# Optimization experiments

Hardware: AMD Instinct MI355X
Metric: run time of the kernel (lower is better)

Reference implementation:

```python
import jax, jax.numpy as jnp
import numpy as np
from jax import lax

N_CLASS, EMB, HID = 32000, 512, 1024
BATCH, SEQ = 64, 256


def _run_lstm(xs, h0, c0, Wg, Wgh, bg, Wi, Wih, bi, Wf, Wfh, bf, Wo, Woh, bo):
    # xs: [T, B, D_in]; weights stored [D_in, H] so step is x @ W (== Linear)
    def step(carry, x):
        h, c = carry
        g = jnp.tanh(x @ Wg + h @ Wgh + bg)
        i = jax.nn.sigmoid(x @ Wi + h @ Wih + bi)
        f = jax.nn.sigmoid(x @ Wf + h @ Wfh + bf)
        o = jax.nn.sigmoid(x @ Wo + h @ Woh + bo)
        c = c * f + g * i
        h = jnp.tanh(c) * o
        return (h, c), h
    (hT, cT), hs = lax.scan(step, (h0, c0), xs)
    return hs, hT


def setup_inputs() -> dict:
    key = jax.random.key(0)
    ks = jax.random.split(key, 32)
    s_e, s_h = 1.0 / np.sqrt(EMB), 1.0 / np.sqrt(HID)
    d = {}
    d["X"] = jax.random.randint(ks[0], (BATCH, SEQ), 0, N_CLASS)
    d["C"] = jax.random.normal(ks[1], (N_CLASS, EMB), jnp.float32)
    # layer 1 (input dim EMB)
    names1 = ["W1", "W_xi", "W_xf", "W_xo"]
    names1h = ["W2", "W_hi", "W_hf", "W_ho"]
    for j, n in enumerate(names1):
        d[n] = jax.random.normal(ks[2 + j], (EMB, HID), jnp.float32) * s_e
    for j, n in enumerate(names1h):
        d[n] = jax.random.normal(ks[6 + j], (HID, HID), jnp.float32) * s_h
    for n in ["b1", "b_i", "b_f", "b_o"]:
        d[n] = jnp.ones((HID,), jnp.float32)
    # layer 2 (input dim HID)
    names2 = ["W1_y", "W_xi_y", "W_xf_y", "W_xo_y", "W2_y", "W_hi_y", "W_hf_y", "W_ho_y"]
    for j, n in enumerate(names2):
        d[n] = jax.random.normal(ks[10 + j], (HID, HID), jnp.float32) * s_h
    for n in ["b1_y", "b_i_y", "b_f_y", "b_o_y"]:
        d[n] = jnp.ones((HID,), jnp.float32)
    d["W3"] = jax.random.normal(ks[20], (HID, N_CLASS), jnp.float32) * s_h
    d["b2"] = jnp.ones((N_CLASS,), jnp.float32)
    # torch code uses torch.randn initial states each call; materialize them
    d["h0"] = jax.random.normal(ks[21], (BATCH, HID), jnp.float32)
    d["c0"] = jax.random.normal(ks[22], (BATCH, HID), jnp.float32)
    d["h0_y"] = jax.random.normal(ks[23], (BATCH, HID), jnp.float32)
    d["c0_y"] = jax.random.normal(ks[24], (BATCH, HID), jnp.float32)
    return d


def reference(X, C, W1, W_xi, W_xf, W_xo, W2, W_hi, W_hf, W_ho,
              b1, b_i, b_f, b_o,
              W1_y, W_xi_y, W_xf_y, W_xo_y, W2_y, W_hi_y, W_hf_y, W_ho_y,
              b1_y, b_i_y, b_f_y, b_o_y, W3, b2, h0, c0, h0_y, c0_y):
    xs = jnp.transpose(C[X], (1, 0, 2))  # [T, B, EMB]
    hs, _ = _run_lstm(xs, h0, c0, W1, W2, b1, W_xi, W_hi, b_i,
                      W_xf, W_hf, b_f, W_xo, W_ho, b_o)
    _, hT_y = _run_lstm(hs, h0_y, c0_y, W1_y, W2_y, b1_y, W_xi_y, W_hi_y, b_i_y,
                        W_xf_y, W_hf_y, b_f_y, W_xo_y, W_ho_y, b_o_y)
    return hT_y @ W3 + b2  # [B, N_CLASS]
```

## Files before the change

kernel.cpp:

```cpp
#include <hip/hip_runtime.h>
#include <hip/hip_bf16.h>


typedef __attribute__((ext_vector_type(8))) short s16x8;
typedef __attribute__((ext_vector_type(4))) float f32x4;
typedef unsigned long long u64;

#define N_CLASS 32000
#define EMB 512
#define HID 1024
#define BATCH 64
#define SEQ 256
#define NG4 4096

#define PIN(v) asm volatile("" : "+v"(v))

static __device__ __forceinline__ short f2bf(float x) {
  __hip_bfloat16 h = __float2bfloat16(x);
  return *reinterpret_cast<short*>(&h);
}
static __device__ __forceinline__ float bf2f(short x) {
  __hip_bfloat16 h = *reinterpret_cast<__hip_bfloat16*>(&x);
  return __bfloat162float(h);
}
static __device__ __forceinline__ float fsigm(float x) {
  return __builtin_amdgcn_rcpf(1.f + __expf(-x));
}
static __device__ __forceinline__ float ftanh(float x) {
  return 2.f * __builtin_amdgcn_rcpf(1.f + __expf(-2.f * x)) - 1.f;
}

__global__ void k_conv_w4(const float* __restrict__ Wg, const float* __restrict__ Wi,
                          const float* __restrict__ Wf, const float* __restrict__ Wo,
                          short* __restrict__ sw, int K) {
  int i = blockIdx.x * 256 + threadIdx.x;
  int k8 = i >> 10, j = i & 1023;
  if (k8 >= (K >> 3)) return;
  const float* W = blockIdx.z == 0 ? Wg : blockIdx.z == 1 ? Wi : blockIdx.z == 2 ? Wf : Wo;
  s16x8 v;
#pragma unroll
  for (int e = 0; e < 8; ++e) v[e] = f2bf(W[(size_t)(k8 * 8 + e) * 1024 + j]);
  *(s16x8*)(sw + ((size_t)k8 * NG4 + blockIdx.z * 1024 + j) * 8) = v;
}

__global__ void k_bcat(const float* __restrict__ b0, const float* __restrict__ b1,
                       const float* __restrict__ b2, const float* __restrict__ b3,
                       float* __restrict__ dst) {
  int i = blockIdx.x * 256 + threadIdx.x;
  const float* s = (i >> 10) == 0 ? b0 : (i >> 10) == 1 ? b1 : (i >> 10) == 2 ? b2 : b3;
  dst[i] = s[i & 1023];
}

__global__ void k_f2bf(const float* __restrict__ src, short* __restrict__ dst, int n) {
  int i = blockIdx.x * 256 + threadIdx.x;
  if (i < n) dst[i] = f2bf(src[i]);
}

__global__ void k_embed(const int* __restrict__ X, const float* __restrict__ C,
                        short* __restrict__ xs) {
  int r = blockIdx.x;
  int t = r >> 6, b = r & 63;
  int idx = X[b * SEQ + t];
  const float* src = C + (size_t)idx * EMB;
  float2 v = *(const float2*)(src + threadIdx.x * 2);
  short* dst = xs + (size_t)r * EMB + threadIdx.x * 2;
  dst[0] = f2bf(v.x);
  dst[1] = f2bf(v.y);
}

__global__ __launch_bounds__(256) void k_gemx(const short* __restrict__ A,
                                              const short* __restrict__ Bsw,
                                              const float* __restrict__ bias,
                                              u64* __restrict__ Gsw) {
  __shared__ short lds[4096 * 8];
  int tid = threadIdx.x;
  int n0 = blockIdx.x * 64;
  for (int cid = tid; cid < 4096; cid += 256) {
    int k8 = cid >> 6, nl = cid & 63;
    *(s16x8*)(lds + (size_t)cid * 8) = *(const s16x8*)(Bsw + ((size_t)k8 * NG4 + n0 + nl) * 8);
  }
  __syncthreads();
  int lane = tid & 63, wid = tid >> 6;
  int l15 = lane & 15, l4 = lane >> 4;
  int ms = wid >> 1, ns = wid & 1;
  for (int m0 = blockIdx.y * 64; m0 < SEQ * BATCH; m0 += gridDim.y * 64) {
    f32x4 acc[2][2];
#pragma unroll
    for (int i = 0; i < 2; ++i)
#pragma unroll
      for (int j = 0; j < 2; ++j) acc[i][j] = (f32x4){0.f, 0.f, 0.f, 0.f};
    const short* a0p = A + (size_t)(m0 + ms * 32 + l15) * EMB + l4 * 8;
    const short* a1p = a0p + (size_t)16 * EMB;
#pragma unroll 4
    for (int kc = 0; kc < 16; ++kc) {
      s16x8 av0 = *(const s16x8*)(a0p + kc * 32);
      s16x8 av1 = *(const s16x8*)(a1p + kc * 32);
#pragma unroll
      for (int j = 0; j < 2; ++j) {
        s16x8 bv = *(const s16x8*)(lds + (size_t)((kc * 4 + l4) * 64 + ns * 32 + j * 16 + l15) * 8);
        acc[0][j] = __builtin_amdgcn_mfma_f32_16x16x32_bf16(av0, bv, acc[0][j], 0, 0, 0);
        acc[1][j] = __builtin_amdgcn_mfma_f32_16x16x32_bf16(av1, bv, acc[1][j], 0, 0, 0);
      }
    }
    int t = m0 >> 6;
#pragma unroll
    for (int i = 0; i < 2; ++i)
#pragma unroll
      for (int j = 0; j < 2; ++j) {
        int grp = ms * 2 + i;
        int colg = n0 + ns * 32 + j * 16 + l15;
        float bv = bias[colg];
        int q = colg >> 10, nslc = (colg >> 4) & 63;
        u64 pk = 0;
#pragma unroll
        for (int e = 0; e < 4; ++e)
          pk |= (u64)(unsigned short)f2bf(acc[i][j][e] + bv) << (16 * e);
        size_t slot = ((((size_t)t * 4 + grp) * 64 + nslc) * 4 + q) * 64 + l4 * 16 + l15;
        Gsw[slot] = pk;
      }
  }
}

__global__ __launch_bounds__(512) __attribute__((amdgpu_waves_per_eu(2, 2))) void k_mega(
    const u64* __restrict__ G64, const short* __restrict__ Wh1sw,
    const short* __restrict__ Wx2sw, const short* __restrict__ Wh2sw,
    const float* __restrict__ bc2, u64* __restrict__ h1ex, u64* __restrict__ h2ex,
    const float* __restrict__ c0, const float* __restrict__ c0y,
    u64* __restrict__ hTy, unsigned* __restrict__ flags) {
  __shared__ short a_lds[2 * 16 * 1024];
  __shared__ f32x4 xch[8][64];
  const int tid = threadIdx.x;
  const int lane = tid & 63, W = tid >> 6;
  const int wv = W & 3, khalf = W >> 2;
  const int l15 = lane & 15, l4 = lane >> 4;
  const int xcd = (int)blockIdx.x & 7;
  const int group = xcd >> 1;
  const int nsl = ((((int)blockIdx.x >> 3) << 1) | (xcd & 1));
  const int col = (l15 >> 2) * 1024 + nsl * 16 + wv * 4 + (l15 & 3);

  s16x8 b1r[16], bxr[16], b2r[16];
#pragma unroll
  for (int j = 0; j < 16; ++j) {
    size_t o = ((size_t)((khalf * 16 + j) * 4 + l4) * NG4 + col) * 8;
    b1r[j] = *(const s16x8*)(Wh1sw + o);
    PIN(b1r[j]);
  }
#pragma unroll
  for (int j = 0; j < 16; ++j) {
    size_t o = ((size_t)((khalf * 16 + j) * 4 + l4) * NG4 + col) * 8;
    bxr[j] = *(const s16x8*)(Wx2sw + o);
    PIN(bxr[j]);
  }
#pragma unroll
  for (int j = 0; j < 16; ++j) {
    size_t o = ((size_t)((khalf * 16 + j) * 4 + l4) * NG4 + col) * 8;
    b2r[j] = *(const s16x8*)(Wh2sw + o);
    PIN(b2r[j]);
  }
  const float bias2 = bc2[col];
  float cv[4];
#pragma unroll
  for (int e = 0; e < 4; ++e) {
    int gi = (group * 16 + l4 * 4 + e) * HID + nsl * 16 + wv * 4 + (l15 & 3);
    cv[e] = (W < 4 ? c0 : c0y)[gi];
  }
  unsigned* arr = flags;
  const int srow = tid >> 5, sc5 = tid & 31;
  const int exrow = (group * 16 + srow) * 256;
  const size_t gbase =
      (((size_t)group * 64 + nsl) * 4 + (l15 >> 2)) * 64 + l4 * 16 + wv * 4 + (l15 & 3);
  u64 gcur = (W < 4) ? G64[gbase] : 0;
  u64 gnext = 0;
  const int gsrc = l4 * 16 + (l15 & 3);
  const int psrc = ((l15 >> 2) << 4) + ((l15 & 3) << 2);
  const int swzm = (l15 & 7) << 4;
  const int abase = l15 * 2048 + khalf * 1024 + l4 * 16;

  for (int r = 0; r <= 256; ++r) {
    if (W < 4 && r + 1 < 256) gnext = G64[gbase + (size_t)(r + 1) * 65536];
    if (r > 0) {
      if (tid < 64) {
        unsigned* p = arr + ((group << 6) + tid) * 32;
        while (__hip_atomic_load(p, __ATOMIC_RELAXED, __HIP_MEMORY_SCOPE_AGENT) <
               (unsigned)r) {
        }
      }
      __syncthreads();
      asm volatile("" ::: "memory");
    }
    {
      const int slot = (r + 1) & 1;
      const u64* s1 = h1ex + slot * 16384 + exrow;
      const u64* s2 = h2ex + slot * 16384 + exrow;
#pragma unroll
      for (int i = 0; i < 8; ++i) {
        int chunk = sc5 + (i << 5);
        u64 v1 = __hip_atomic_load(s1 + chunk, __ATOMIC_RELAXED, __HIP_MEMORY_SCOPE_AGENT);
        u64 v2 = __hip_atomic_load(s2 + chunk, __ATOMIC_RELAXED, __HIP_MEMORY_SCOPE_AGENT);
        int bo = (srow * 2048 + chunk * 8) ^ ((srow & 7) << 4);
        *(u64*)((char*)a_lds + bo) = v1;
        *(u64*)((char*)a_lds + 32768 + bo) = v2;
      }
    }
    __syncthreads();

    f32x4 p1, p2a, p2b;
    if (W < 4) {
#pragma unroll
      for (int e = 0; e < 4; ++e)
        p1[e] = __uint_as_float((unsigned)((gcur >> (16 * e)) & 0xffffu) << 16);
      p2a = (f32x4){0.f, 0.f, 0.f, 0.f};
    } else {
      p1 = (f32x4){0.f, 0.f, 0.f, 0.f};
      p2a = (f32x4){bias2, bias2, bias2, bias2};
    }
    p2b = (f32x4){0.f, 0.f, 0.f, 0.f};
#pragma unroll
    for (int j = 0; j < 16; ++j) {
      int o = (abase + j * 64) ^ swzm;
      s16x8 a1 = *(const s16x8*)((const char*)a_lds + o);
      s16x8 a2 = *(const s16x8*)((const char*)a_lds + 32768 + o);
      p1 = __builtin_amdgcn_mfma_f32_16x16x32_bf16(a1, b1r[j], p1, 0, 0, 0);
      p2a = __builtin_amdgcn_mfma_f32_16x16x32_bf16(a1, bxr[j], p2a, 0, 0, 0);
      p2b = __builtin_amdgcn_mfma_f32_16x16x32_bf16(a2, b2r[j], p2b, 0, 0, 0);
    }
    f32x4 p2 = p2a + p2b;
    if (W < 4) {
      if (r >= 1) xch[W][lane] = p2;
    } else {
      if (r < 256) xch[W][lane] = p1;
    }
    __syncthreads();

    if (W < 4) {
      if (r < 256) {
        f32x4 po = xch[W + 4][lane];
        f32x4 acc = p1 + po;
        float hh0, hh1, hh2, hh3;
#pragma unroll
        for (int e = 0; e < 4; ++e) {
          float xg = __shfl(acc[e], gsrc + 0);
          float xi = __shfl(acc[e], gsrc + 4);
          float xf = __shfl(acc[e], gsrc + 8);
          float xo = __shfl(acc[e], gsrc + 12);
          float cn = cv[e] * fsigm(xf) + ftanh(xg) * fsigm(xi);
          cv[e] = cn;
          float hv = ftanh(cn) * fsigm(xo);
          if (e == 0) hh0 = hv;
          else if (e == 1) hh1 = hv;
          else if (e == 2) hh2 = hv;
          else hh3 = hv;
        }
        int rr = l15 >> 2;
        float hexp = rr == 0 ? hh0 : rr == 1 ? hh1 : rr == 2 ? hh2 : hh3;
        float p0 = __shfl(hexp, psrc + 0);
        float p1s = __shfl(hexp, psrc + 1);
        float p2s = __shfl(hexp, psrc + 2);
        float p3s = __shfl(hexp, psrc + 3);
        if (lane < 16) {
          u64 pk = (u64)(unsigned short)f2bf(p0) | ((u64)(unsigned short)f2bf(p1s) << 16) |
                   ((u64)(unsigned short)f2bf(p2s) << 32) |
                   ((u64)(unsigned short)f2bf(p3s) << 48);
          __hip_atomic_store(
              h1ex + (r & 1) * 16384 + (group * 16 + lane) * 256 + nsl * 4 + wv, pk,
              __ATOMIC_RELAXED, __HIP_MEMORY_SCOPE_AGENT);
        }
      }
    } else {
      if (r >= 1) {
        f32x4 po = xch[W - 4][lane];
        f32x4 acc = p2 + po;
        float hh0, hh1, hh2, hh3;
#pragma unroll
        for (int e = 0; e < 4; ++e) {
          float xg = __shfl(acc[e], gsrc + 0);
          float xi = __shfl(acc[e], gsrc + 4);
          float xf = __shfl(acc[e], gsrc + 8);
          float xo = __shfl(acc[e], gsrc + 12);
          float cn = cv[e] * fsigm(xf) + ftanh(xg) * fsigm(xi);
          cv[e] = cn;
          float hv = ftanh(cn) * fsigm(xo);
          if (e == 0) hh0 = hv;
          else if (e == 1) hh1 = hv;
          else if (e == 2) hh2 = hv;
          else hh3 = hv;
        }
        int rr = l15 >> 2;
        float hexp = rr == 0 ? hh0 : rr == 1 ? hh1 : rr == 2 ? hh2 : hh3;
        float p0 = __shfl(hexp, psrc + 0);
        float p1s = __shfl(hexp, psrc + 1);
        float p2s = __shfl(hexp, psrc + 2);
        float p3s = __shfl(hexp, psrc + 3);
        if (lane < 16) {
          u64 pk = (u64)(unsigned short)f2bf(p0) | ((u64)(unsigned short)f2bf(p1s) << 16) |
                   ((u64)(unsigned short)f2bf(p2s) << 32) |
                   ((u64)(unsigned short)f2bf(p3s) << 48);
          int idx = (group * 16 + lane) * 256 + nsl * 4 + wv;
          if (r < 256)
            __hip_atomic_store(h2ex + (r & 1) * 16384 + idx, pk, __ATOMIC_RELAXED,
                               __HIP_MEMORY_SCOPE_AGENT);
          else
            hTy[idx] = pk;
        }
      }
    }

    if (r < 256) {
      asm volatile("s_waitcnt vmcnt(0)" ::: "memory");
      __syncthreads();
      if (tid == 0)
        __hip_atomic_store(arr + ((group << 6) + nsl) * 32, (unsigned)(r + 1),
                           __ATOMIC_RELAXED, __HIP_MEMORY_SCOPE_AGENT);
    }
    gcur = gnext;
  }
}

__global__ __launch_bounds__(256) void k_final(const short* __restrict__ hT,
                                               const float* __restrict__ W3,
                                               float* __restrict__ partial) {
  __shared__ float hst[64][64];
  int tid = threadIdx.x;
  int n = blockIdx.x * 256 + tid;
  int kbase = blockIdx.y * 512;
  float acc[64];
#pragma unroll
  for (int i = 0; i < 64; ++i) acc[i] = 0.f;
  int bb = tid >> 2, part = tid & 3;
  for (int kc = 0; kc < 512; kc += 64) {
    __syncthreads();
    s16x8 v0 = *(const s16x8*)(hT + bb * HID + kbase + kc + part * 16);
    s16x8 v1 = *(const s16x8*)(hT + bb * HID + kbase + kc + part * 16 + 8);
#pragma unroll
    for (int e = 0; e < 8; ++e) {
      hst[part * 16 + e][bb] = bf2f(v0[e]);
      hst[part * 16 + 8 + e][bb] = bf2f(v1[e]);
    }
    __syncthreads();
    for (int k = 0; k < 64; ++k) {
      float wv = W3[(size_t)(kbase + kc + k) * N_CLASS + n];
      const float4* hp = (const float4*)&hst[k][0];
#pragma unroll
      for (int b4 = 0; b4 < 16; ++b4) {
        float4 h4 = hp[b4];
        acc[b4 * 4 + 0] += h4.x * wv;
        acc[b4 * 4 + 1] += h4.y * wv;
        acc[b4 * 4 + 2] += h4.z * wv;
        acc[b4 * 4 + 3] += h4.w * wv;
      }
    }
  }
#pragma unroll
  for (int b = 0; b < 64; ++b)
    partial[((size_t)blockIdx.y * 64 + b) * N_CLASS + n] = acc[b];
}

__global__ void k_fincomb(const float* __restrict__ partial, const float* __restrict__ b2,
                          float* __restrict__ out) {
  int n = blockIdx.x * 256 + threadIdx.x;
  int b = blockIdx.y;
  out[(size_t)b * N_CLASS + n] =
      partial[(size_t)b * N_CLASS + n] + partial[((size_t)64 + b) * N_CLASS + n] + b2[n];
}

extern "C" void kernel_launch(void* const* d_in, const int* in_sizes, int n_in, void* d_out,
                              int out_size, void* d_ws, size_t ws_size, hipStream_t stream) {
  (void)in_sizes; (void)n_in; (void)out_size; (void)ws_size;
  const int* X = (const int*)d_in[0];
  const float* C = (const float*)d_in[1];
  const float* W1 = (const float*)d_in[2];
  const float* W_xi = (const float*)d_in[3];
  const float* W_xf = (const float*)d_in[4];
  const float* W_xo = (const float*)d_in[5];
  const float* W2 = (const float*)d_in[6];
  const float* W_hi = (const float*)d_in[7];
  const float* W_hf = (const float*)d_in[8];
  const float* W_ho = (const float*)d_in[9];
  const float* b1 = (const float*)d_in[10];
  const float* b_i = (const float*)d_in[11];
  const float* b_f = (const float*)d_in[12];
  const float* b_o = (const float*)d_in[13];
  const float* W1_y = (const float*)d_in[14];
  const float* W_xi_y = (const float*)d_in[15];
  const float* W_xf_y = (const float*)d_in[16];
  const float* W_xo_y = (const float*)d_in[17];
  const float* W2_y = (const float*)d_in[18];
  const float* W_hi_y = (const float*)d_in[19];
  const float* W_hf_y = (const float*)d_in[20];
  const float* W_ho_y = (const float*)d_in[21];
  const float* b1_y = (const float*)d_in[22];
  const float* b_i_y = (const float*)d_in[23];
  const float* b_f_y = (const float*)d_in[24];
  const float* b_o_y = (const float*)d_in[25];
  const float* W3 = (const float*)d_in[26];
  const float* b2 = (const float*)d_in[27];
  const float* h0 = (const float*)d_in[28];
  const float* c0 = (const float*)d_in[29];
  const float* h0_y = (const float*)d_in[30];
  const float* c0_y = (const float*)d_in[31];

  char* w = (char*)d_ws;
  size_t off = 0;
  auto take = [&](size_t bytes) {
    char* p = w + off;
    off += (bytes + 255) & ~(size_t)255;
    return p;
  };
  short* wx1 = (short*)take(64UL * NG4 * 8 * 2);
  short* wh1 = (short*)take(128UL * NG4 * 8 * 2);
  short* wx2 = (short*)take(128UL * NG4 * 8 * 2);
  short* wh2 = (short*)take(128UL * NG4 * 8 * 2);
  short* xs = (short*)take((size_t)SEQ * BATCH * EMB * 2);
  u64* G1sw = (u64*)take((size_t)SEQ * 65536 * 8);
  float* bc1 = (float*)take(NG4 * 4);
  float* bc2 = (float*)take(NG4 * 4);
  u64* h1ex = (u64*)take(2UL * 16384 * 8);
  u64* h2ex = (u64*)take(2UL * 16384 * 8);
  u64* hTy = (u64*)take(16384UL * 8);
  unsigned* flags = (unsigned*)take(65536);

  hipMemsetAsync(flags, 0, 65536, stream);
  k_bcat<<<16, 256, 0, stream>>>(b1, b_i, b_f, b_o, bc1);
  k_bcat<<<16, 256, 0, stream>>>(b1_y, b_i_y, b_f_y, b_o_y, bc2);
  k_f2bf<<<256, 256, 0, stream>>>(h0, (short*)h1ex + 65536, BATCH * HID);
  k_f2bf<<<256, 256, 0, stream>>>(h0_y, (short*)h2ex, BATCH * HID);
  k_conv_w4<<<dim3(256, 1, 4), 256, 0, stream>>>(W1, W_xi, W_xf, W_xo, wx1, 512);
  k_conv_w4<<<dim3(512, 1, 4), 256, 0, stream>>>(W2, W_hi, W_hf, W_ho, wh1, 1024);
  k_conv_w4<<<dim3(512, 1, 4), 256, 0, stream>>>(W1_y, W_xi_y, W_xf_y, W_xo_y, wx2, 1024);
  k_conv_w4<<<dim3(512, 1, 4), 256, 0, stream>>>(W2_y, W_hi_y, W_hf_y, W_ho_y, wh2, 1024);
  k_embed<<<SEQ * BATCH, 256, 0, stream>>>(X, C, xs);
  k_gemx<<<dim3(64, 16), 256, 0, stream>>>(xs, wx1, bc1, G1sw);
  k_mega<<<256, 512, 0, stream>>>(G1sw, wh1, wx2, wh2, bc2, h1ex, h2ex, c0, c0_y, hTy,
                                  flags);
  float* partial = (float*)G1sw;
  k_final<<<dim3(125, 2), 256, 0, stream>>>((const short*)hTy, W3, partial);
  k_fincomb<<<dim3(125, 64), 256, 0, stream>>>(partial, b2, (float*)d_out);
}
```

Measured before the change: 2.443 ms.

## Split LSTM layers into decoupled wave groups with separate flag pipelines

Restructures the persistent recurrent kernel so layer 1 and layer 2 run on separate wave groups (4 waves for layer 1, 8 for layer 2) with their own global step flags. They synchronise through LDS atomic counters instead of block-wide barriers, so layer 2 can lag layer 1 and the two recurrences pipeline. Each wave now holds the full K=1024 weight slice for one gate in registers and gate math is done per element with LDS exchange. This adds spin-wait complexity, higher register pressure at 768 threads, and a risk of ordering bugs between the LDS counters and global flags.

```diff
diff --git a/kernel.cpp b/kernel.cpp
--- a/kernel.cpp
+++ b/kernel.cpp
@@ -28,6 +28,17 @@
 }
 static __device__ __forceinline__ float ftanh(float x) {
   return 2.f * __builtin_amdgcn_rcpf(1.f + __expf(-2.f * x)) - 1.f;
+}
+static __device__ __forceinline__ u64 pack4(float a, float b, float c, float d) {
+  return (u64)(unsigned short)f2bf(a) | ((u64)(unsigned short)f2bf(b) << 16) |
+         ((u64)(unsigned short)f2bf(c) << 32) | ((u64)(unsigned short)f2bf(d) << 48);
+}
+static __device__ __forceinline__ void wgadd(unsigned* c) {
+  __hip_atomic_fetch_add(c, 1u, __ATOMIC_RELEASE, __HIP_MEMORY_SCOPE_WORKGROUP);
+}
+static __device__ __forceinline__ void wgwait(unsigned* c, unsigned tgt) {
+  while (__hip_atomic_load(c, __ATOMIC_ACQUIRE, __HIP_MEMORY_SCOPE_WORKGROUP) < tgt) {
+  }
 }
 
 __global__ void k_conv_w4(const float* __restrict__ Wg, const float* __restrict__ Wi,
@@ -121,198 +132,206 @@
   }
 }
 
-__global__ __launch_bounds__(512) __attribute__((amdgpu_waves_per_eu(2, 2))) void k_mega(
+__global__ __launch_bounds__(768) __attribute__((amdgpu_waves_per_eu(3))) void k_mega(
     const u64* __restrict__ G64, const short* __restrict__ Wh1sw,
     const short* __restrict__ Wx2sw, const short* __restrict__ Wh2sw,
     const float* __restrict__ bc2, u64* __restrict__ h1ex, u64* __restrict__ h2ex,
     const float* __restrict__ c0, const float* __restrict__ c0y,
     u64* __restrict__ hTy, unsigned* __restrict__ flags) {
-  __shared__ short a_lds[2 * 16 * 1024];
-  __shared__ f32x4 xch[8][64];
+  __shared__ short A1[16 * 1024];
+  __shared__ float gx1[4][16][16];
+  __shared__ short B1[16 * 1024];
+  __shared__ short B2[16 * 1024];
+  __shared__ float xch2[2][4][16][16];
+  __shared__ unsigned cnt[16];
+
   const int tid = threadIdx.x;
   const int lane = tid & 63, W = tid >> 6;
-  const int wv = W & 3, khalf = W >> 2;
-  const int l15 = lane & 15, l4 = lane >> 4;
   const int xcd = (int)blockIdx.x & 7;
   const int group = xcd >> 1;
   const int nsl = ((((int)blockIdx.x >> 3) << 1) | (xcd & 1));
-  const int col = (l15 >> 2) * 1024 + nsl * 16 + wv * 4 + (l15 & 3);
-
-  s16x8 b1r[16], bxr[16], b2r[16];
-#pragma unroll
-  for (int j = 0; j < 16; ++j) {
-    size_t o = ((size_t)((khalf * 16 + j) * 4 + l4) * NG4 + col) * 8;
-    b1r[j] = *(const s16x8*)(Wh1sw + o);
-    PIN(b1r[j]);
-  }
-#pragma unroll
-  for (int j = 0; j < 16; ++j) {
-    size_t o = ((size_t)((khalf * 16 + j) * 4 + l4) * NG4 + col) * 8;
-    bxr[j] = *(const s16x8*)(Wx2sw + o);
-    PIN(bxr[j]);
-  }
-#pragma unroll
-  for (int j = 0; j < 16; ++j) {
-    size_t o = ((size_t)((khalf * 16 + j) * 4 + l4) * NG4 + col) * 8;
-    b2r[j] = *(const s16x8*)(Wh2sw + o);
-    PIN(b2r[j]);
-  }
-  const float bias2 = bc2[col];
-  float cv[4];
-#pragma unroll
-  for (int e = 0; e < 4; ++e) {
-    int gi = (group * 16 + l4 * 4 + e) * HID + nsl * 16 + wv * 4 + (l15 & 3);
-    cv[e] = (W < 4 ? c0 : c0y)[gi];
-  }
-  unsigned* arr = flags;
-  const int srow = tid >> 5, sc5 = tid & 31;
-  const int exrow = (group * 16 + srow) * 256;
-  const size_t gbase =
-      (((size_t)group * 64 + nsl) * 4 + (l15 >> 2)) * 64 + l4 * 16 + wv * 4 + (l15 & 3);
-  u64 gcur = (W < 4) ? G64[gbase] : 0;
-  u64 gnext = 0;
-  const int gsrc = l4 * 16 + (l15 & 3);
-  const int psrc = ((l15 >> 2) << 4) + ((l15 & 3) << 2);
+  if (tid < 16) cnt[tid] = 0u;
+  __syncthreads();
+
+  unsigned* flags1 = flags;
+  unsigned* flags2 = flags + 8192;
+  const int l15 = lane & 15, l4 = lane >> 4;
+  const int abase = l15 * 2048 + l4 * 16;
   const int swzm = (l15 & 7) << 4;
-  const int abase = l15 * 2048 + khalf * 1024 + l4 * 16;
-
-  for (int r = 0; r <= 256; ++r) {
-    if (W < 4 && r + 1 < 256) gnext = G64[gbase + (size_t)(r + 1) * 65536];
-    if (r > 0) {
-      if (tid < 64) {
-        unsigned* p = arr + ((group << 6) + tid) * 32;
-        while (__hip_atomic_load(p, __ATOMIC_RELAXED, __HIP_MEMORY_SCOPE_AGENT) <
-               (unsigned)r) {
+
+  if (W < 4) {
+    const int q = W;
+    s16x8 b1r[32];
+#pragma unroll
+    for (int j = 0; j < 32; ++j) {
+      b1r[j] = *(const s16x8*)(Wh1sw + ((size_t)(j * 4 + l4) * NG4 + q * 1024 + nsl * 16 + l15) * 8);
+      PIN(b1r[j]);
+    }
+    const int b_ = tid >> 4, d_ = tid & 15;
+    float c1 = c0[(group * 16 + b_) * HID + nsl * 16 + d_];
+    const size_t gbase = (((size_t)group * 64 + nsl) * 4 + q) * 64 + l4 * 16 + l15;
+    u64 gcur = G64[gbase], gnext = 0;
+    unsigned* f1 = flags1 + (group << 6) * 32;
+    for (int r = 0; r < 256; ++r) {
+      if (r + 1 < 256) gnext = G64[gbase + (size_t)(r + 1) * 65536];
+      if (r > 0) {
+        if (W == 0) {
+          unsigned* p = f1 + lane * 32;
+          while (__hip_atomic_load(p, __ATOMIC_RELAXED, __HIP_MEMORY_SCOPE_AGENT) <
+                 (unsigned)r)
+            __builtin_amdgcn_s_sleep(1);
+          if (lane == 0) wgadd(&cnt[4]);
         }
-      }
-      __syncthreads();
+        wgwait(&cnt[4], (unsigned)r);
+        asm volatile("" ::: "memory");
+      }
+      wgwait(&cnt[1], (unsigned)(4 * r));
+      {
+        const u64* s1 = h1ex + ((r + 1) & 1) * 16384 + (size_t)(group * 16 + b_) * 256;
+#pragma unroll
+        for (int i = 0; i < 16; ++i) {
+          int chunk = d_ + (i << 4);
+          u64 v = __hip_atomic_load(s1 + chunk, __ATOMIC_RELAXED, __HIP_MEMORY_SCOPE_AGENT);
+          *(u64*)((char*)A1 + ((b_ * 2048 + chunk * 8) ^ ((b_ & 7) << 4))) = v;
+        }
+      }
+      if (lane == 0) wgadd(&cnt[0]);
+      wgwait(&cnt[0], (unsigned)(4 * (r + 1)));
+      f32x4 ca, cb;
+#pragma unroll
+      for (int e = 0; e < 4; ++e)
+        ca[e] = __uint_as_float((unsigned)((gcur >> (16 * e)) & 0xffffu) << 16);
+      cb = (f32x4){0.f, 0.f, 0.f, 0.f};
+#pragma unroll
+      for (int j = 0; j < 32; j += 2) {
+        s16x8 x0 = *(const s16x8*)((const char*)A1 + ((abase + j * 64) ^ swzm));
+        s16x8 x1 = *(const s16x8*)((const char*)A1 + ((abase + (j + 1) * 64) ^ swzm));
+        ca = __builtin_amdgcn_mfma_f32_16x16x32_bf16(x0, b1r[j], ca, 0, 0, 0);
+        cb = __builtin_amdgcn_mfma_f32_16x16x32_bf16(x1, b1r[j + 1], cb, 0, 0, 0);
+      }
+      f32x4 acc = ca + cb;
+#pragma unroll
+      for (int e = 0; e < 4; ++e) gx1[q][l4 * 4 + e][l15] = acc[e];
+      if (lane == 0) wgadd(&cnt[1]);
+      wgwait(&cnt[1], (unsigned)(4 * (r + 1)));
+      float sg = gx1[0][b_][d_], si = gx1[1][b_][d_];
+      float sf = gx1[2][b_][d_], so = gx1[3][b_][d_];
+      c1 = c1 * fsigm(sf) + ftanh(sg) * fsigm(si);
+      float h = ftanh(c1) * fsigm(so);
+      int basel = lane & 60;
+      float p0 = __shfl(h, basel + 0), p1v = __shfl(h, basel + 1);
+      float p2v = __shfl(h, basel + 2), p3v = __shfl(h, basel + 3);
+      if ((lane & 3) == 0) {
+        u64 pk = pack4(p0, p1v, p2v, p3v);
+        __hip_atomic_store(
+            h1ex + (r & 1) * 16384 + (size_t)(group * 16 + b_) * 256 + nsl * 4 + (d_ >> 2),
+            pk, __ATOMIC_RELAXED, __HIP_MEMORY_SCOPE_AGENT);
+      }
+      asm volatile("s_waitcnt vmcnt(0)" ::: "memory");
+      if (lane == 0) wgadd(&cnt[7]);
+      if (tid == 0) {
+        wgwait(&cnt[7], (unsigned)(4 * (r + 1)));
+        wgwait(&cnt[2], (unsigned)(8 * r));
+        __hip_atomic_store(f1 + nsl * 32, (unsigned)(r + 1), __ATOMIC_RELAXED,
+                           __HIP_MEMORY_SCOPE_AGENT);
+      }
+      gcur = gnext;
+    }
+  } else {
+    const int w2 = W - 4;
+    const int q = w2 & 3, mat = w2 >> 2;
+    const short* Wsrc = mat ? Wh2sw : Wx2sw;
+    s16x8 wq[32];
+#pragma unroll
+    for (int j = 0; j < 32; ++j) {
+      wq[j] = *(const s16x8*)(Wsrc + ((size_t)(j * 4 + l4) * NG4 + q * 1024 + nsl * 16 + l15) * 8);
+      PIN(wq[j]);
+    }
+    const int t2 = tid - 256;
+    const int srow = t2 >> 5, sc5 = t2 & 31;
+    const int t2a = tid - 512;
+    const int b_ = (t2a >> 4) & 15, d_ = t2a & 15;
+    float c2 = 0.f, bz0 = 0.f, bz1 = 0.f, bz2 = 0.f, bz3 = 0.f;
+    if (w2 >= 4) {
+      c2 = c0y[(group * 16 + b_) * HID + nsl * 16 + d_];
+      bz0 = bc2[nsl * 16 + d_];
+      bz1 = bc2[1024 + nsl * 16 + d_];
+      bz2 = bc2[2048 + nsl * 16 + d_];
+      bz3 = bc2[3072 + nsl * 16 + d_];
+    }
+    unsigned* f1 = flags1 + (group << 6) * 32;
+    unsigned* f2 = flags2 + (group << 6) * 32;
+    const short* Bmine = mat ? B2 : B1;
+    for (int s = 0; s < 256; ++s) {
+      if (W == 4) {
+        unsigned* p1p = f1 + lane * 32;
+        unsigned* p2p = f2 + lane * 32;
+        while (__hip_atomic_load(p1p, __ATOMIC_RELAXED, __HIP_MEMORY_SCOPE_AGENT) <
+                   (unsigned)(s + 1) ||
+               __hip_atomic_load(p2p, __ATOMIC_RELAXED, __HIP_MEMORY_SCOPE_AGENT) <
+                   (unsigned)s)
+          __builtin_amdgcn_s_sleep(1);
+        if (lane == 0) wgadd(&cnt[5]);
+      }
+      wgwait(&cnt[5], (unsigned)(s + 1));
       asm volatile("" ::: "memory");
-    }
-    {
-      const int slot = (r + 1) & 1;
-      const u64* s1 = h1ex + slot * 16384 + exrow;
-      const u64* s2 = h2ex + slot * 16384 + exrow;
-#pragma unroll
-      for (int i = 0; i < 8; ++i) {
-        int chunk = sc5 + (i << 5);
-        u64 v1 = __hip_atomic_load(s1 + chunk, __ATOMIC_RELAXED, __HIP_MEMORY_SCOPE_AGENT);
-        u64 v2 = __hip_atomic_load(s2 + chunk, __ATOMIC_RELAXED, __HIP_MEMORY_SCOPE_AGENT);
-        int bo = (srow * 2048 + chunk * 8) ^ ((srow & 7) << 4);
-        *(u64*)((char*)a_lds + bo) = v1;
-        *(u64*)((char*)a_lds + 32768 + bo) = v2;
-      }
-    }
-    __syncthreads();
-
-    f32x4 p1, p2a, p2b;
-    if (W < 4) {
-#pragma unroll
-      for (int e = 0; e < 4; ++e)
-        p1[e] = __uint_as_float((unsigned)((gcur >> (16 * e)) & 0xffffu) << 16);
-      p2a = (f32x4){0.f, 0.f, 0.f, 0.f};
-    } else {
-      p1 = (f32x4){0.f, 0.f, 0.f, 0.f};
-      p2a = (f32x4){bias2, bias2, bias2, bias2};
-    }
-    p2b = (f32x4){0.f, 0.f, 0.f, 0.f};
-#pragma unroll
-    for (int j = 0; j < 16; ++j) {
-      int o = (abase + j * 64) ^ swzm;
-      s16x8 a1 = *(const s16x8*)((const char*)a_lds + o);
-      s16x8 a2 = *(const s16x8*)((const char*)a_lds + 32768 + o);
-      p1 = __builtin_amdgcn_mfma_f32_16x16x32_bf16(a1, b1r[j], p1, 0, 0, 0);
-      p2a = __builtin_amdgcn_mfma_f32_16x16x32_bf16(a1, bxr[j], p2a, 0, 0, 0);
-      p2b = __builtin_amdgcn_mfma_f32_16x16x32_bf16(a2, b2r[j], p2b, 0, 0, 0);
-    }
-    f32x4 p2 = p2a + p2b;
-    if (W < 4) {
-      if (r >= 1) xch[W][lane] = p2;
-    } else {
-      if (r < 256) xch[W][lane] = p1;
-    }
-    __syncthreads();
-
-    if (W < 4) {
-      if (r < 256) {
-        f32x4 po = xch[W + 4][lane];
-        f32x4 acc = p1 + po;
-        float hh0, hh1, hh2, hh3;
-#pragma unroll
-        for (int e = 0; e < 4; ++e) {
-          float xg = __shfl(acc[e], gsrc + 0);
-          float xi = __shfl(acc[e], gsrc + 4);
-          float xf = __shfl(acc[e], gsrc + 8);
-          float xo = __shfl(acc[e], gsrc + 12);
-          float cn = cv[e] * fsigm(xf) + ftanh(xg) * fsigm(xi);
-          cv[e] = cn;
-          float hv = ftanh(cn) * fsigm(xo);
-          if (e == 0) hh0 = hv;
-          else if (e == 1) hh1 = hv;
-          else if (e == 2) hh2 = hv;
-          else hh3 = hv;
+      wgwait(&cnt[3], (unsigned)(8 * s));
+      {
+        const u64* sB1 = h1ex + (s & 1) * 16384 + (size_t)(group * 16 + srow) * 256;
+        const u64* sB2 = h2ex + ((s + 1) & 1) * 16384 + (size_t)(group * 16 + srow) * 256;
+#pragma unroll
+        for (int i = 0; i < 8; ++i) {
+          int chunk = sc5 + (i << 5);
+          u64 v1 = __hip_atomic_load(sB1 + chunk, __ATOMIC_RELAXED, __HIP_MEMORY_SCOPE_AGENT);
+          u64 v2 = __hip_atomic_load(sB2 + chunk, __ATOMIC_RELAXED, __HIP_MEMORY_SCOPE_AGENT);
+          int bo = (srow * 2048 + chunk * 8) ^ ((srow & 7) << 4);
+          *(u64*)((char*)B1 + bo) = v1;
+          *(u64*)((char*)B2 + bo) = v2;
         }
-        int rr = l15 >> 2;
-        float hexp = rr == 0 ? hh0 : rr == 1 ? hh1 : rr == 2 ? hh2 : hh3;
-        float p0 = __shfl(hexp, psrc + 0);
-        float p1s = __shfl(hexp, psrc + 1);
-        float p2s = __shfl(hexp, psrc + 2);
-        float p3s = __shfl(hexp, psrc + 3);
-        if (lane < 16) {
-          u64 pk = (u64)(unsigned short)f2bf(p0) | ((u64)(unsigned short)f2bf(p1s) << 16) |
-                   ((u64)(unsigned short)f2bf(p2s) << 32) |
-                   ((u64)(unsigned short)f2bf(p3s) << 48);
-          __hip_atomic_store(
-              h1ex + (r & 1) * 16384 + (group * 16 + lane) * 256 + nsl * 4 + wv, pk,
-              __ATOMIC_RELAXED, __HIP_MEMORY_SCOPE_AGENT);
-        }
-      }
-    } else {
-      if (r >= 1) {
-        f32x4 po = xch[W - 4][lane];
-        f32x4 acc = p2 + po;
-        float hh0, hh1, hh2, hh3;
-#pragma unroll
-        for (int e = 0; e < 4; ++e) {
-          float xg = __shfl(acc[e], gsrc + 0);
-          float xi = __shfl(acc[e], gsrc + 4);
-          float xf = __shfl(acc[e], gsrc + 8);
-          float xo = __shfl(acc[e], gsrc + 12);
-          float cn = cv[e] * fsigm(xf) + ftanh(xg) * fsigm(xi);
-          cv[e] = cn;
-          float hv = ftanh(cn) * fsigm(xo);
-          if (e == 0) hh0 = hv;
-          else if (e == 1) hh1 = hv;
-          else if (e == 2) hh2 = hv;
-          else hh3 = hv;
-        }
-        int rr = l15 >> 2;
-        float hexp = rr == 0 ? hh0 : rr == 1 ? hh1 : rr == 2 ? hh2 : hh3;
-        float p0 = __shfl(hexp, psrc + 0);
-        float p1s = __shfl(hexp, psrc + 1);
-        float p2s = __shfl(hexp, psrc + 2);
-        float p3s = __shfl(hexp, psrc + 3);
-        if (lane < 16) {
-          u64 pk = (u64)(unsigned short)f2bf(p0) | ((u64)(unsigned short)f2bf(p1s) << 16) |
-                   ((u64)(unsigned short)f2bf(p2s) << 32) |
-                   ((u64)(unsigned short)f2bf(p3s) << 48);
-          int idx = (group * 16 + lane) * 256 + nsl * 4 + wv;
-          if (r < 256)
-            __hip_atomic_store(h2ex + (r & 1) * 16384 + idx, pk, __ATOMIC_RELAXED,
+      }
+      if (lane == 0) wgadd(&cnt[2]);
+      wgwait(&cnt[2], (unsigned)(8 * (s + 1)));
+      f32x4 ca = (f32x4){0.f, 0.f, 0.f, 0.f}, cb = (f32x4){0.f, 0.f, 0.f, 0.f};
+#pragma unroll
+      for (int j = 0; j < 32; j += 2) {
+        s16x8 x0 = *(const s16x8*)((const char*)Bmine + ((abase + j * 64) ^ swzm));
+        s16x8 x1 = *(const s16x8*)((const char*)Bmine + ((abase + (j + 1) * 64) ^ swzm));
+        ca = __builtin_amdgcn_mfma_f32_16x16x32_bf16(x0, wq[j], ca, 0, 0, 0);
+        cb = __builtin_amdgcn_mfma_f32_16x16x32_bf16(x1, wq[j + 1], cb, 0, 0, 0);
+      }
+      f32x4 acc = ca + cb;
+#pragma unroll
+      for (int e = 0; e < 4; ++e) xch2[mat][q][l4 * 4 + e][l15] = acc[e];
+      if (lane == 0) wgadd(&cnt[3]);
+      if (w2 >= 4) {
+        wgwait(&cnt[3], (unsigned)(8 * (s + 1)));
+        float sg = xch2[0][0][b_][d_] + xch2[1][0][b_][d_] + bz0;
+        float si = xch2[0][1][b_][d_] + xch2[1][1][b_][d_] + bz1;
+        float sf = xch2[0][2][b_][d_] + xch2[1][2][b_][d_] + bz2;
+        float so = xch2[0][3][b_][d_] + xch2[1][3][b_][d_] + bz3;
+        c2 = c2 * fsigm(sf) + ftanh(sg) * fsigm(si);
+        float h = ftanh(c2) * fsigm(so);
+        int basel = lane & 60;
+        float p0 = __shfl(h, basel + 0), p1v = __shfl(h, basel + 1);
+        float p2v = __shfl(h, basel + 2), p3v = __shfl(h, basel + 3);
+        if ((lane & 3) == 0) {
+          u64 pk = pack4(p0, p1v, p2v, p3v);
+          size_t idx = (size_t)(group * 16 + b_) * 256 + nsl * 4 + (d_ >> 2);
+          if (s < 255)
+            __hip_atomic_store(h2ex + (s & 1) * 16384 + idx, pk, __ATOMIC_RELAXED,
                                __HIP_MEMORY_SCOPE_AGENT);
           else
             hTy[idx] = pk;
         }
-      }
-    }
-
-    if (r < 256) {
-      asm volatile("s_waitcnt vmcnt(0)" ::: "memory");
-      __syncthreads();
-      if (tid == 0)
-        __hip_atomic_store(arr + ((group << 6) + nsl) * 32, (unsigned)(r + 1),
-                           __ATOMIC_RELAXED, __HIP_MEMORY_SCOPE_AGENT);
-    }
-    gcur = gnext;
+        asm volatile("s_waitcnt vmcnt(0)" ::: "memory");
+        if (lane == 0) wgadd(&cnt[6]);
+        if (tid == 512) {
+          wgwait(&cnt[6], (unsigned)(4 * (s + 1)));
+          __hip_atomic_store(f2 + nsl * 32, (unsigned)(s + 1), __ATOMIC_RELAXED,
+                             __HIP_MEMORY_SCOPE_AGENT);
+        }
+      }
+    }
   }
 }
 
@@ -423,14 +442,14 @@
   k_bcat<<<16, 256, 0, stream>>>(b1, b_i, b_f, b_o, bc1);
   k_bcat<<<16, 256, 0, stream>>>(b1_y, b_i_y, b_f_y, b_o_y, bc2);
   k_f2bf<<<256, 256, 0, stream>>>(h0, (short*)h1ex + 65536, BATCH * HID);
-  k_f2bf<<<256, 256, 0, stream>>>(h0_y, (short*)h2ex, BATCH * HID);
+  k_f2bf<<<256, 256, 0, stream>>>(h0_y, (short*)h2ex + 65536, BATCH * HID);
   k_conv_w4<<<dim3(256, 1, 4), 256, 0, stream>>>(W1, W_xi, W_xf, W_xo, wx1, 512);
   k_conv_w4<<<dim3(512, 1, 4), 256, 0, stream>>>(W2, W_hi, W_hf, W_ho, wh1, 1024);
   k_conv_w4<<<dim3(512, 1, 4), 256, 0, stream>>>(W1_y, W_xi_y, W_xf_y, W_xo_y, wx2, 1024);
   k_conv_w4<<<dim3(512, 1, 4), 256, 0, stream>>>(W2_y, W_hi_y, W_hf_y, W_ho_y, wh2, 1024);
   k_embed<<<SEQ * BATCH, 256, 0, stream>>>(X, C, xs);
   k_gemx<<<dim3(64, 16), 256, 0, stream>>>(xs, wx1, bc1, G1sw);
-  k_mega<<<256, 512, 0, stream>>>(G1sw, wh1, wx2, wh2, bc2, h1ex, h2ex, c0, c0_y, hTy,
+  k_mega<<<256, 768, 0, stream>>>(G1sw, wh1, wx2, wh2, bc2, h1ex, h2ex, c0, c0_y, hTy,
                                   flags);
   float* partial = (float*)G1sw;
   k_final<<<dim3(125, 2), 256, 0, stream>>>((const short*)hTy, W3, partial);
```

Result: slower. 3.948 ms (+61.6%).
